# Kernel optimization log

Hardware: AMD Instinct MI355X
Metric: run time of the kernel (lower is better)

The kernel has to match this reference:

```python
import jax, jax.numpy as jnp
import numpy as np

N_NODES = 100000
N_EDGES = 1600000
IN_C, HID_C, OUT_C, N_CLS = 128, 128, 128, 40


def setup_inputs() -> dict:
    key = jax.random.key(0)
    ks = jax.random.split(key, 10)
    x = jax.random.normal(ks[0], (N_NODES, IN_C), dtype=jnp.float32)
    edge_index = jax.random.randint(ks[1], (2, N_EDGES), 0, N_NODES, dtype=jnp.int64)
    s = 1.0 / np.sqrt(IN_C)
    W_self1 = jax.random.uniform(ks[2], (IN_C, HID_C), jnp.float32, -s, s)
    W_neigh1 = jax.random.uniform(ks[3], (IN_C, HID_C), jnp.float32, -s, s)
    b1 = jnp.zeros((HID_C,), jnp.float32)
    s2 = 1.0 / np.sqrt(HID_C)
    W_self2 = jax.random.uniform(ks[4], (HID_C, OUT_C), jnp.float32, -s2, s2)
    W_neigh2 = jax.random.uniform(ks[5], (HID_C, OUT_C), jnp.float32, -s2, s2)
    b2 = jnp.zeros((OUT_C,), jnp.float32)
    s3 = 1.0 / np.sqrt(OUT_C)
    W_cls = jax.random.uniform(ks[6], (OUT_C, N_CLS), jnp.float32, -s3, s3)
    b_cls = jax.random.uniform(ks[7], (N_CLS,), jnp.float32, -s3, s3)
    return dict(x=x, edge_index=edge_index, W_self1=W_self1, W_neigh1=W_neigh1, b1=b1,
                W_self2=W_self2, W_neigh2=W_neigh2, b2=b2, W_cls=W_cls, b_cls=b_cls)


def _mean_agg(h, src, dst, n_nodes):
    # sum of in-neighbor features per destination node, then divide by in-degree
    sums = jax.ops.segment_sum(h[src], dst, num_segments=n_nodes)  # [N, F]
    deg = jax.ops.segment_sum(jnp.ones(src.shape[0], h.dtype), dst, num_segments=n_nodes)
    return sums / jnp.maximum(deg, 1.0)[:, None]


def _sage_conv(h, src, dst, W_self, W_neigh, b):
    # DGL mean SAGEConv: fc_self(h) + fc_neigh(mean_neigh(h)) + bias
    h_neigh = _mean_agg(h, src, dst, h.shape[0])
    return h @ W_self + h_neigh @ W_neigh + b


def reference(x, edge_index, W_self1, W_neigh1, b1, W_self2, W_neigh2, b2, W_cls, b_cls):
    src, dst = edge_index[0], edge_index[1]
    h = jax.nn.relu(_sage_conv(x, src, dst, W_self1, W_neigh1, b1))
    h = jax.nn.relu(_sage_conv(h, src, dst, W_self2, W_neigh2, b2))
    return h @ W_cls + b_cls
```

## Files before the change

### kernel.cpp

```cpp
#include <hip/hip_runtime.h>

#define N_NODES 100000
#define N_EDGES 1600000
#define C 128
#define NCLS 40
#define NBUCK 196
#define BCAP 12288

typedef _Float16 half8 __attribute__((ext_vector_type(8)));
typedef float f32x4 __attribute__((ext_vector_type(4)));
typedef float f32x16 __attribute__((ext_vector_type(16)));


__global__ __launch_bounds__(256) void bucket_scatter_k(const int* __restrict__ src,
    const int* __restrict__ dst, int* __restrict__ bucket_cnt, int* __restrict__ bucketArr) {
  __shared__ int lh[NBUCK], lbase[NBUCK], lcur[NBUCK];
  int tid = threadIdx.x;
  for (int i = tid; i < NBUCK; i += 256) { lh[i] = 0; lcur[i] = 0; }
  __syncthreads();
  int base = blockIdx.x * 4096;
  int bmax = min(base + 4096, N_EDGES);
  int dreg[16];
  int nk = 0;
  for (int e = base + tid; e < bmax; e += 256) dreg[nk++] = dst[e];
  for (int k = 0; k < nk; k++) atomicAdd(&lh[dreg[k] >> 9], 1);
  __syncthreads();
  for (int i = tid; i < NBUCK; i += 256)
    lbase[i] = lh[i] ? atomicAdd(&bucket_cnt[i], lh[i]) : 0;
  __syncthreads();
  nk = 0;
  for (int e = base + tid; e < bmax; e += 256) {
    int d = dreg[nk++];
    int b = d >> 9, loc = d & 511;
    int p = lbase[b] + atomicAdd(&lcur[b], 1);
    if (p < BCAP) bucketArr[(size_t)b * BCAP + p] = (src[e] << 9) | loc;
  }
}

__global__ __launch_bounds__(256) void bucket_sort_k(const int* __restrict__ bucketArr,
    const int* __restrict__ bucket_cnt, int* __restrict__ rp, int* __restrict__ csr) {
  __shared__ int pref[NBUCK + 1];
  __shared__ int hist[512], offs[512], curs[512];
  __shared__ int wpart[4];
  __shared__ int lsrc[BCAP];
  int b = blockIdx.x, tid = threadIdx.x;
  int lane = tid & 63, wid = tid >> 6;

  {
    int v = (tid < NBUCK) ? min(bucket_cnt[tid], BCAP) : 0;
    int inc = v;
    for (int d = 1; d < 64; d <<= 1) { int y = __shfl_up(inc, d, 64); if (lane >= d) inc += y; }
    if (lane == 63) wpart[wid] = inc;
    __syncthreads();
    int woff = 0;
    for (int q = 0; q < wid; q++) woff += wpart[q];
    int ex = woff + inc - v;
    if (tid < NBUCK) pref[tid] = ex;
    if (tid == NBUCK - 1) pref[NBUCK] = ex + v;
    __syncthreads();
  }
  int base = pref[b];
  int cnt = min(bucket_cnt[b], BCAP);
  if (b == 0 && tid == 0) rp[N_NODES] = pref[NBUCK];
  __syncthreads();

  for (int i = tid; i < 512; i += 256) hist[i] = 0;
  __syncthreads();
  for (int i = tid; i < cnt; i += 256)
    atomicAdd(&hist[bucketArr[(size_t)b * BCAP + i] & 511], 1);
  __syncthreads();
  int a0 = hist[2 * tid], a1 = hist[2 * tid + 1];
  int s = a0 + a1;
  int inc = s;
  for (int d = 1; d < 64; d <<= 1) { int y = __shfl_up(inc, d, 64); if (lane >= d) inc += y; }
  if (lane == 63) wpart[wid] = inc;
  __syncthreads();
  int woff = 0;
  for (int q = 0; q < wid; q++) woff += wpart[q];
  int ex = woff + inc - s;
  offs[2 * tid] = ex; offs[2 * tid + 1] = ex + a0;
  curs[2 * tid] = ex; curs[2 * tid + 1] = ex + a0;
  __syncthreads();
  for (int i = tid; i < 512; i += 256) {
    int gn = b * 512 + i;
    if (gn < N_NODES) rp[gn] = base + offs[i];
  }
  for (int i = tid; i < cnt; i += 256) {
    int packed = bucketArr[(size_t)b * BCAP + i];
    int p = atomicAdd(&curs[packed & 511], 1);
    lsrc[p] = packed >> 9;
  }
  __syncthreads();
  for (int i = tid; i < cnt; i += 256) csr[base + i] = lsrc[i];
}


__global__ __launch_bounds__(256) void prep_k(const float* __restrict__ x,
    const float* __restrict__ Ws1, const float* __restrict__ Wn1,
    const float* __restrict__ Ws2, const float* __restrict__ Wn2,
    const float* __restrict__ Wc, const float* __restrict__ bc,
    _Float16* __restrict__ xh, _Float16* __restrict__ WT1, _Float16* __restrict__ WT2,
    _Float16* __restrict__ WcT, float* __restrict__ bcf) {
  int bid = blockIdx.x, tid = threadIdx.x;
  if (bid < 6250) {
    int i = bid * 256 + tid;
    float4 v0 = *(const float4*)(x + (size_t)i * 8);
    float4 v1 = *(const float4*)(x + (size_t)i * 8 + 4);
    half8 o;
    o[0] = (_Float16)v0.x; o[1] = (_Float16)v0.y; o[2] = (_Float16)v0.z; o[3] = (_Float16)v0.w;
    o[4] = (_Float16)v1.x; o[5] = (_Float16)v1.y; o[6] = (_Float16)v1.z; o[7] = (_Float16)v1.w;
    *(half8*)(xh + (size_t)i * 8) = o;
    return;
  }
  int b = bid - 6250, k = tid;
  if (b < 128) {
    float v = (k < 128) ? Ws1[k * 128 + b] : Wn1[(k - 128) * 128 + b];
    WT1[b * 256 + k] = (_Float16)v;
  } else if (b < 256) {
    int n = b - 128;
    float v = (k < 128) ? Ws2[k * 128 + n] : Wn2[(k - 128) * 128 + n];
    WT2[n * 256 + k] = (_Float16)v;
  } else if (k < 128) {
    int c = b - 256;
    float v = (c < NCLS) ? Wc[k * NCLS + c] : 0.f;
    WcT[c * C + k] = (_Float16)v;
    if (k == 0) bcf[c] = (c < NCLS) ? bc[c] : 0.f;
  }
}


__global__ __launch_bounds__(256) void agg_mean_h_k(const _Float16* __restrict__ feat,
    const int* __restrict__ rp, const int* __restrict__ csr, _Float16* __restrict__ out) {
  int w = threadIdx.x >> 6;
  int node = blockIdx.x * 4 + w;
  int lane = threadIdx.x & 63;
  int g = lane >> 4, lr = lane & 15;
  int beg = rp[node], end = rp[node + 1];
  int deg = end - beg;
  int csrv = (beg + lane < end) ? csr[beg + lane] : 0;

  half8 h0 = {}, h1 = {}, h2 = {}, h3 = {};
  int dcap = min(deg, 64);
  int nfull = dcap >> 2;
  int it = 0;
  for (; it + 4 <= nfull; it += 4) {
    int e0 = __shfl(csrv, (it << 2) + g, 64);
    int e1 = __shfl(csrv, ((it + 1) << 2) + g, 64);
    int e2 = __shfl(csrv, ((it + 2) << 2) + g, 64);
    int e3 = __shfl(csrv, ((it + 3) << 2) + g, 64);
    h0 += *(const half8*)(feat + (size_t)e0 * C + lr * 8);
    h1 += *(const half8*)(feat + (size_t)e1 * C + lr * 8);
    h2 += *(const half8*)(feat + (size_t)e2 * C + lr * 8);
    h3 += *(const half8*)(feat + (size_t)e3 * C + lr * 8);
  }
  for (; it < nfull; it++) {
    int e0 = __shfl(csrv, (it << 2) + g, 64);
    h0 += *(const half8*)(feat + (size_t)e0 * C + lr * 8);
  }
  int rem = dcap & 3;
  if (rem) {
    int e0 = __shfl(csrv, (nfull << 2) + g, 64);
    if (g < rem) h1 += *(const half8*)(feat + (size_t)e0 * C + lr * 8);
  }
  for (int j = beg + 64; j < end; j += 4) {
    if (j + g < end) {
      int e0 = csr[j + g];
      h2 += *(const half8*)(feat + (size_t)e0 * C + lr * 8);
    }
  }

  float acc[8];
#pragma unroll
  for (int q = 0; q < 8; q++)
    acc[q] = ((float)h0[q] + (float)h1[q]) + ((float)h2[q] + (float)h3[q]);
#pragma unroll
  for (int q = 0; q < 8; q++) {
    float v = acc[q];
    v += __shfl_xor(v, 16, 64);
    v += __shfl_xor(v, 32, 64);
    acc[q] = v;
  }
  if (g == 0) {
    float inv = 1.0f / fmaxf((float)deg, 1.0f);
    half8 o;
#pragma unroll
    for (int q = 0; q < 8; q++) o[q] = (_Float16)(acc[q] * inv);
    *(half8*)(out + (size_t)node * C + lr * 8) = o;
  }
}


template <bool CLS>
__global__ __launch_bounds__(256, 2) void sage_gemm_ws_k(
    const _Float16* __restrict__ Xs, const _Float16* __restrict__ Xn,
    const _Float16* __restrict__ WT, const float* __restrict__ bias,
    const _Float16* __restrict__ WcT, const float* __restrict__ bcf,
    _Float16* __restrict__ out_h, float* __restrict__ out_cls) {
  __shared__ _Float16 cbuf[32][136];
  int tid = threadIdx.x, lane = tid & 63, wid = tid >> 6;
  int l31 = lane & 31, l5 = lane >> 5;
  int col0 = wid * 32;
  size_t row0 = (size_t)blockIdx.x * 32;

  half8 a[16], b[16];
#pragma unroll
  for (int ks = 0; ks < 8; ks++) {
    a[ks] = *(const half8*)(Xs + (row0 + l31) * C + ks * 16 + l5 * 8);
    b[ks] = *(const half8*)(WT + (size_t)(col0 + l31) * 256 + ks * 16 + l5 * 8);
  }
#pragma unroll
  for (int ks = 8; ks < 16; ks++) {
    a[ks] = *(const half8*)(Xn + (row0 + l31) * C + (ks - 8) * 16 + l5 * 8);
    b[ks] = *(const half8*)(WT + (size_t)(col0 + l31) * 256 + ks * 16 + l5 * 8);
  }
  float bcol = bias[col0 + l31];
  __builtin_amdgcn_sched_barrier(0);

  f32x16 acc = {};
#pragma unroll
  for (int ks = 0; ks < 16; ks++)
    acc = __builtin_amdgcn_mfma_f32_32x32x16_f16(a[ks], b[ks], acc, 0, 0, 0);

#pragma unroll
  for (int q = 0; q < 16; q++) {
    int row = (q & 3) + 8 * (q >> 2) + 4 * l5;
    float v = fmaxf(acc[q] + bcol, 0.f);
    cbuf[row][col0 + l31] = (_Float16)v;
  }
  __syncthreads();

  if (!CLS) {
#pragma unroll
    for (int p = 0; p < 2; p++) {
      int chunk = tid + p * 256;
      int r = chunk >> 4, cg = chunk & 15;
      half8 v = *(const half8*)&cbuf[r][cg * 8];
      *(half8*)(out_h + (row0 + r) * C + cg * 8) = v;
    }
  } else if (wid < 2) {
    int lr16 = lane & 15, lk = lane >> 4;
    f32x4 cacc[3] = {};
#pragma unroll
    for (int ks = 0; ks < 4; ks++) {
      half8 av = *(const half8*)(&cbuf[wid * 16 + lr16][ks * 32 + lk * 8]);
#pragma unroll
      for (int nf = 0; nf < 3; nf++) {
        half8 bf = *(const half8*)(WcT + (size_t)(nf * 16 + lr16) * C + ks * 32 + lk * 8);
        cacc[nf] = __builtin_amdgcn_mfma_f32_16x16x32_f16(av, bf, cacc[nf], 0, 0, 0);
      }
    }
#pragma unroll
    for (int nf = 0; nf < 3; nf++) {
      int c = nf * 16 + lr16;
      if (c < NCLS) {
#pragma unroll
        for (int q = 0; q < 4; q++) {
          size_t r = row0 + wid * 16 + lk * 4 + q;
          out_cls[r * NCLS + c] = cacc[nf][q] + bcf[c];
        }
      }
    }
  }
}


extern "C" void kernel_launch(void* const* d_in, const int* in_sizes, int n_in,
                              void* d_out, int out_size, void* d_ws, size_t ws_size,
                              hipStream_t stream) {
  (void)in_sizes; (void)n_in; (void)out_size; (void)ws_size;
  const float* x   = (const float*)d_in[0];
  const int*   ei  = (const int*)d_in[1];
  const float* Ws1 = (const float*)d_in[2];
  const float* Wn1 = (const float*)d_in[3];
  const float* b1  = (const float*)d_in[4];
  const float* Ws2 = (const float*)d_in[5];
  const float* Wn2 = (const float*)d_in[6];
  const float* b2  = (const float*)d_in[7];
  const float* Wc  = (const float*)d_in[8];
  const float* bc  = (const float*)d_in[9];
  const int* src = ei;
  const int* dst = ei + N_EDGES;

  char* ws = (char*)d_ws;
  size_t off = 0;
  auto alloc = [&](size_t bytes) {
    void* p = ws + off;
    off = (off + bytes + 255) & ~(size_t)255;
    return p;
  };
  int*      bucket_cnt  = (int*)alloc((size_t)NBUCK * 4);
  int*      bucketArr   = (int*)alloc((size_t)NBUCK * BCAP * 4);
  int*      rp          = (int*)alloc((size_t)(N_NODES + 1) * 4);
  int*      csr         = (int*)alloc((size_t)N_EDGES * 4);
  _Float16* hA          = (_Float16*)alloc((size_t)N_NODES * C * 2);
  _Float16* hB          = (_Float16*)alloc((size_t)N_NODES * C * 2);
  _Float16* hC          = (_Float16*)alloc((size_t)N_NODES * C * 2);
  _Float16* WT1         = (_Float16*)alloc((size_t)C * 256 * 2);
  _Float16* WT2         = (_Float16*)alloc((size_t)C * 256 * 2);
  _Float16* WcT         = (_Float16*)alloc((size_t)48 * C * 2);
  float*    bcf         = (float*)alloc(48 * 4);
  float* outf = (float*)d_out;

  hipMemsetAsync(bucket_cnt, 0, (size_t)NBUCK * 4, stream);
  bucket_scatter_k<<<(N_EDGES + 4095) / 4096, 256, 0, stream>>>(src, dst, bucket_cnt, bucketArr);
  bucket_sort_k<<<NBUCK, 256, 0, stream>>>(bucketArr, bucket_cnt, rp, csr);

  prep_k<<<6554, 256, 0, stream>>>(x, Ws1, Wn1, Ws2, Wn2, Wc, bc, hA, WT1, WT2, WcT, bcf);

  agg_mean_h_k<<<N_NODES / 4, 256, 0, stream>>>(hA, rp, csr, hB);
  sage_gemm_ws_k<false><<<3125, 256, 0, stream>>>(hA, hB, WT1, b1, nullptr, nullptr, hC, nullptr);
  agg_mean_h_k<<<N_NODES / 4, 256, 0, stream>>>(hC, rp, csr, hB);
  sage_gemm_ws_k<true><<<3125, 256, 0, stream>>>(hC, hB, WT2, b2, WcT, bcf, nullptr, outf);
}
```

Before: 371.0 us.

## Stage GEMM A tile in swizzled LDS and prepack weights in MFMA fragment order

The fused SAGE GEMM used to have every wave load the full 32-row A tile (self and neighbor features) straight from global memory. Now the block loads that tile once, cooperatively and coalesced, into an XOR-swizzled LDS buffer, and each wave reads its MFMA A fragments from LDS. The weights are prepacked in prep_k into the lane order the fragments need, so B loads are contiguous. Fewer registers allow raising launch bounds to three blocks per SM. The cost is an extra syncthreads and 16KB of LDS per block, which may limit occupancy.

```diff
diff --git a/kernel.cpp b/kernel.cpp
--- a/kernel.cpp
+++ b/kernel.cpp
@@ -99,7 +99,7 @@
     const float* __restrict__ Ws1, const float* __restrict__ Wn1,
     const float* __restrict__ Ws2, const float* __restrict__ Wn2,
     const float* __restrict__ Wc, const float* __restrict__ bc,
-    _Float16* __restrict__ xh, _Float16* __restrict__ WT1, _Float16* __restrict__ WT2,
+    _Float16* __restrict__ xh, _Float16* __restrict__ WTp1, _Float16* __restrict__ WTp2,
     _Float16* __restrict__ WcT, float* __restrict__ bcf) {
   int bid = blockIdx.x, tid = threadIdx.x;
   if (bid < 6250) {
@@ -115,11 +115,13 @@
   int b = bid - 6250, k = tid;
   if (b < 128) {
     float v = (k < 128) ? Ws1[k * 128 + b] : Wn1[(k - 128) * 128 + b];
-    WT1[b * 256 + k] = (_Float16)v;
+    int cb = b >> 5, l31 = b & 31, ks = k >> 4, l5 = (k >> 3) & 1, j = k & 7;
+    WTp1[(size_t)(cb * 16 + ks) * 512 + (l5 * 32 + l31) * 8 + j] = (_Float16)v;
   } else if (b < 256) {
     int n = b - 128;
     float v = (k < 128) ? Ws2[k * 128 + n] : Wn2[(k - 128) * 128 + n];
-    WT2[n * 256 + k] = (_Float16)v;
+    int cb = n >> 5, l31 = n & 31, ks = k >> 4, l5 = (k >> 3) & 1, j = k & 7;
+    WTp2[(size_t)(cb * 16 + ks) * 512 + (l5 * 32 + l31) * 8 + j] = (_Float16)v;
   } else if (k < 128) {
     int c = b - 256;
     float v = (c < NCLS) ? Wc[k * NCLS + c] : 0.f;
@@ -191,35 +193,43 @@
 
 
 template <bool CLS>
-__global__ __launch_bounds__(256, 2) void sage_gemm_ws_k(
+__global__ __launch_bounds__(256, 3) void sage_gemm_lds_k(
     const _Float16* __restrict__ Xs, const _Float16* __restrict__ Xn,
-    const _Float16* __restrict__ WT, const float* __restrict__ bias,
+    const _Float16* __restrict__ WTp, const float* __restrict__ bias,
     const _Float16* __restrict__ WcT, const float* __restrict__ bcf,
     _Float16* __restrict__ out_h, float* __restrict__ out_cls) {
+  __shared__ _Float16 As[32 * 256];
   __shared__ _Float16 cbuf[32][136];
   int tid = threadIdx.x, lane = tid & 63, wid = tid >> 6;
   int l31 = lane & 31, l5 = lane >> 5;
   int col0 = wid * 32;
   size_t row0 = (size_t)blockIdx.x * 32;
 
-  half8 a[16], b[16];
-#pragma unroll
-  for (int ks = 0; ks < 8; ks++) {
-    a[ks] = *(const half8*)(Xs + (row0 + l31) * C + ks * 16 + l5 * 8);
-    b[ks] = *(const half8*)(WT + (size_t)(col0 + l31) * 256 + ks * 16 + l5 * 8);
-  }
-#pragma unroll
-  for (int ks = 8; ks < 16; ks++) {
-    a[ks] = *(const half8*)(Xn + (row0 + l31) * C + (ks - 8) * 16 + l5 * 8);
-    b[ks] = *(const half8*)(WT + (size_t)(col0 + l31) * 256 + ks * 16 + l5 * 8);
-  }
+  half8 b[16];
+#pragma unroll
+  for (int ks = 0; ks < 16; ks++)
+    b[ks] = *(const half8*)(WTp + (size_t)(wid * 16 + ks) * 512 + lane * 8);
   float bcol = bias[col0 + l31];
-  __builtin_amdgcn_sched_barrier(0);
+
+#pragma unroll
+  for (int it = 0; it < 4; it++) {
+    int off = it * 4096 + tid * 16;
+    int row = off >> 9;
+    int p = off & 511;
+    int c = p ^ ((row & 7) << 4);
+    const _Float16* srcp = (c < 256) ? (Xs + (row0 + row) * C + (c >> 1))
+                                     : (Xn + (row0 + row) * C + ((c - 256) >> 1));
+    *(half8*)((char*)As + off) = *(const half8*)srcp;
+  }
+  __syncthreads();
 
   f32x16 acc = {};
 #pragma unroll
-  for (int ks = 0; ks < 16; ks++)
-    acc = __builtin_amdgcn_mfma_f32_32x32x16_f16(a[ks], b[ks], acc, 0, 0, 0);
+  for (int ks = 0; ks < 16; ks++) {
+    int phys = (ks * 32 + l5 * 16) ^ ((l31 & 7) << 4);
+    half8 a = *(const half8*)((const char*)As + l31 * 512 + phys);
+    acc = __builtin_amdgcn_mfma_f32_32x32x16_f16(a, b[ks], acc, 0, 0, 0);
+  }
 
 #pragma unroll
   for (int q = 0; q < 16; q++) {
@@ -295,8 +305,8 @@
   _Float16* hA          = (_Float16*)alloc((size_t)N_NODES * C * 2);
   _Float16* hB          = (_Float16*)alloc((size_t)N_NODES * C * 2);
   _Float16* hC          = (_Float16*)alloc((size_t)N_NODES * C * 2);
-  _Float16* WT1         = (_Float16*)alloc((size_t)C * 256 * 2);
-  _Float16* WT2         = (_Float16*)alloc((size_t)C * 256 * 2);
+  _Float16* WTp1        = (_Float16*)alloc((size_t)C * 256 * 2);
+  _Float16* WTp2        = (_Float16*)alloc((size_t)C * 256 * 2);
   _Float16* WcT         = (_Float16*)alloc((size_t)48 * C * 2);
   float*    bcf         = (float*)alloc(48 * 4);
   float* outf = (float*)d_out;
@@ -305,10 +315,10 @@
   bucket_scatter_k<<<(N_EDGES + 4095) / 4096, 256, 0, stream>>>(src, dst, bucket_cnt, bucketArr);
   bucket_sort_k<<<NBUCK, 256, 0, stream>>>(bucketArr, bucket_cnt, rp, csr);
 
-  prep_k<<<6554, 256, 0, stream>>>(x, Ws1, Wn1, Ws2, Wn2, Wc, bc, hA, WT1, WT2, WcT, bcf);
+  prep_k<<<6554, 256, 0, stream>>>(x, Ws1, Wn1, Ws2, Wn2, Wc, bc, hA, WTp1, WTp2, WcT, bcf);
 
   agg_mean_h_k<<<N_NODES / 4, 256, 0, stream>>>(hA, rp, csr, hB);
-  sage_gemm_ws_k<false><<<3125, 256, 0, stream>>>(hA, hB, WT1, b1, nullptr, nullptr, hC, nullptr);
+  sage_gemm_lds_k<false><<<3125, 256, 0, stream>>>(hA, hB, WTp1, b1, nullptr, nullptr, hC, nullptr);
   agg_mean_h_k<<<N_NODES / 4, 256, 0, stream>>>(hC, rp, csr, hB);
-  sage_gemm_ws_k<true><<<3125, 256, 0, stream>>>(hC, hB, WT2, b2, WcT, bcf, nullptr, outf);
-}
+  sage_gemm_lds_k<true><<<3125, 256, 0, stream>>>(hC, hB, WTp2, b2, WcT, bcf, nullptr, outf);
+}
```

Result: faster. 300.2 us (-19.1%).
